# Kernel optimization log

Hardware: AMD Instinct MI355X
Metric: run time of the kernel (lower is better)

The kernel has to match this reference:

```python
import jax, jax.numpy as jnp
import numpy as np

B, N, K, S_IN, S_OUT, C, FD = 32, 325, 20, 12, 12, 10, 64
ALPHA = 0.5  # LeakyReLU negative slope

def leaky(x):
    return jnp.where(x >= 0, x, ALPHA * x)

def setup_inputs() -> dict:
    key = jax.random.key(0)
    ks = jax.random.split(key, 9)
    s = 0.2
    return {
        "fushed_features": jax.random.normal(ks[0], (B, N, FD), jnp.float32),
        "input_data": jax.random.normal(ks[1], (B, N, S_IN), jnp.float32),
        "w_W": jax.random.normal(ks[2], (S_IN, S_OUT), jnp.float32) * s,
        "w_b": jax.random.normal(ks[3], (S_OUT,), jnp.float32) * s,
        "a1_W": jax.random.normal(ks[4], (2 * S_OUT, 4 * S_OUT), jnp.float32) * s,
        "a1_b": jax.random.normal(ks[5], (4 * S_OUT,), jnp.float32) * s,
        "a2_W": jax.random.normal(ks[6], (4 * S_OUT, C), jnp.float32) * s,
        "a2_b": jax.random.normal(ks[7], (C,), jnp.float32) * s,
        "adj_mx_topk_index": jax.random.randint(ks[8], (B, N, K), 0, N),
    }

def reference(fushed_features, input_data, w_W, w_b, a1_W, a1_b, a2_W, a2_b, adj_mx_topk_index):
    # w_net: Linear + LeakyReLU -> wh [B,N,S_OUT]
    wh = leaky(input_data @ w_W + w_b)
    # a_net on cat([wh_i, wh_j]): split first linear to avoid materializing [B,N,N,2*S_OUT]
    hx = wh @ a1_W[:S_OUT]   # contribution of wh_x (row node i)
    hy = wh @ a1_W[S_OUT:]   # contribution of wh_y (col node j)
    hidden = leaky(hx[:, :, None, :] + hy[:, None, :, :] + a1_b)   # [B,N,N,4*S_OUT]
    attention = leaky(hidden @ a2_W + a2_b)                        # [B,N,N,C]
    idx = adj_mx_topk_index                                        # [B,N,K]
    # gather top-k neighbors along dim 2
    idx_c = jnp.broadcast_to(idx[..., None], idx.shape + (attention.shape[-1],))
    attention_mask = jnp.take_along_axis(attention, idx_c, axis=2)  # [B,N,K,C]
    attention_mask = jax.nn.softmax(attention_mask, axis=-1)
    # gather neighbor features: wh_expand_top_k[b,i,k] = wh[b, idx[b,i,k]]
    wh_topk = wh[jnp.arange(wh.shape[0])[:, None, None], idx]       # [B,N,K,S_OUT]
    # output = attention_mask^T @ wh_topk
    output_data = jnp.einsum('bnkc,bnks->bncs', attention_mask, wh_topk)
    # clustering loss on detached neighbor features (cosine similarity)
    wt = jax.lax.stop_gradient(wh_topk)
    wtn = wt / (jnp.linalg.norm(wt, axis=-1, keepdims=True) + 1e-8)
    dist_mat = jnp.einsum('bnks,bnls->bnkl', wtn, wtn)              # [B,N,K,K]
    same = (dist_mat >= 0.5).astype(dist_mat.dtype)
    diff = 1.0 - same
    prob = jnp.einsum('bnkc,bnlc->bnkl', attention_mask, attention_mask)
    prob = jnp.clip(prob, 1e-4, 1.0 - 1e-4)
    logp = jnp.log(prob)
    cl = -(same * logp - diff * logp)
    cluster_loss = (cl.sum((-1, -2)) - jnp.trace(cl, axis1=-2, axis2=-1)).mean()
    return output_data, cluster_loss, dist_mat.mean(), wh.mean()
```

## Files before the change

### kernel.cpp

```cpp
#include <hip/hip_runtime.h>
#include <math.h>

#define Bdim 32
#define Ndim 325
#define Kdim 20
#define Sdim 12
#define Cdim 10
#define Hdim 48
#define NB   (Bdim*Ndim)
#define OUT_SCALARS (NB*Cdim*Sdim)
#define Tpairs (Kdim*(Kdim-1)/2)

#define O_WH  0
#define O_HX  (O_WH + NB*Sdim)
#define O_HY  (O_HX + NB*Hdim)
#define O_PCL (O_HY + NB*Hdim)
#define O_PDS (O_PCL + NB)
#define O_PWH (O_PDS + NB)
#define WS_BASE_FLOATS (O_PWH + NB)

__device__ __forceinline__ float leaky(float x) { return x >= 0.f ? x : 0.5f * x; }

__global__ __launch_bounds__(256)
void node_kernel(const float* __restrict__ x,
                 const float* __restrict__ wW, const float* __restrict__ wb,
                 const float* __restrict__ A1, const float* __restrict__ b1,
                 float* __restrict__ ws)
{
    __shared__ float s_wh[4][Sdim];
    const int slot = threadIdx.x >> 6, lane = threadIdx.x & 63;
    const int node = blockIdx.x * 4 + slot;
    const float* xr = x + (size_t)node * Sdim;

    float v = 0.f;
    if (lane < Sdim) {
        float acc = wb[lane];
        #pragma unroll
        for (int i = 0; i < Sdim; i++) acc += xr[i] * wW[i * Sdim + lane];
        v = leaky(acc);
        s_wh[slot][lane] = v;
        ws[O_WH + (size_t)node * Sdim + lane] = v;
    }
    __syncthreads();

    #pragma unroll
    for (int rep = 0; rep < 2; rep++) {
        const int e = lane + rep * 64;
        if (e < 2 * Hdim) {
            const int which = e / Hdim, d = e - which * Hdim;
            float acc = which ? 0.f : b1[d];
            #pragma unroll
            for (int s = 0; s < Sdim; s++)
                acc += s_wh[slot][s] * A1[(which * Sdim + s) * Hdim + d];
            ws[(which ? O_HY : O_HX) + (size_t)node * Hdim + d] = acc;
        }
    }

    #pragma unroll
    for (int off = 32; off > 0; off >>= 1) v += __shfl_down(v, off);
    if (lane == 0) ws[O_PWH + node] = v;
}

__global__ __launch_bounds__(64)
void bn_kernel(const int* __restrict__ topk,
               const float* __restrict__ A2, const float* __restrict__ b2,
               float* __restrict__ ws, float* __restrict__ out)
{
    __shared__ float s_hxb[Hdim];
    __shared__ float s_A2[Hdim][12];
    __shared__ float s_whj[Kdim][20];
    __shared__ float s_wtn[Kdim][20];
    __shared__ float s_am [Kdim][12];
    __shared__ int   s_idx[Kdim];

    const int t = threadIdx.x, bn = blockIdx.x, b = bn / Ndim;

    if (t < Kdim) s_idx[t] = topk[(size_t)bn * Kdim + t];
    if (t < Hdim) s_hxb[t] = ws[O_HX + (size_t)bn * Hdim + t];
    for (int i = t; i < Hdim * 12; i += 64) {
        const int d = i / 12, c = i - d * 12;
        s_A2[d][c] = (c < Cdim) ? A2[d * Cdim + c] : 0.f;
    }
    __syncthreads();

    if (t < Kdim * 3) {
        const int k = t / 3, q = t - k * 3;
        const float4 v = *(const float4*)(ws + O_WH + ((size_t)b * Ndim + s_idx[k]) * Sdim + q * 4);
        *(float4*)&s_whj[k][q * 4] = v;
    }
    __syncthreads();

    float cl = 0.f, ds = 0.f;

    if (t < 2 * Kdim) {
        const int k = t >> 1, half = t & 1;
        const float4* hy4 = (const float4*)(ws + O_HY + ((size_t)b * Ndim + s_idx[k]) * Hdim) + half * 6;
        float acc[Cdim];
        #pragma unroll
        for (int c = 0; c < Cdim; c++) acc[c] = 0.f;
        #pragma unroll
        for (int q = 0; q < 6; q++) {
            const float4 hv = hy4[q];
            const float hvv[4] = { hv.x, hv.y, hv.z, hv.w };
            #pragma unroll
            for (int i = 0; i < 4; i++) {
                const int d = half * 24 + q * 4 + i;
                const float h = leaky(s_hxb[d] + hvv[i]);
                #pragma unroll
                for (int c = 0; c < Cdim; c++) acc[c] += h * s_A2[d][c];
            }
        }
        float full[Cdim];
        #pragma unroll
        for (int c = 0; c < Cdim; c++) full[c] = acc[c] + __shfl_xor(acc[c], 1);
        if (half == 0) {
            float m = -1e30f;
            #pragma unroll
            for (int c = 0; c < Cdim; c++) { full[c] = leaky(full[c] + b2[c]); m = fmaxf(m, full[c]); }
            float sum = 0.f;
            #pragma unroll
            for (int c = 0; c < Cdim; c++) { full[c] = __expf(full[c] - m); sum += full[c]; }
            const float inv = 1.f / sum;
            #pragma unroll
            for (int c = 0; c < Cdim; c++) s_am[k][c] = full[c] * inv;
            s_am[k][10] = 0.f; s_am[k][11] = 0.f;
        }
    } else if (t < 2 * Kdim + Kdim) {
        const int k = t - 2 * Kdim;
        const float4 w0 = *(const float4*)&s_whj[k][0];
        const float4 w1 = *(const float4*)&s_whj[k][4];
        const float4 w2 = *(const float4*)&s_whj[k][8];
        const float nn = w0.x*w0.x + w0.y*w0.y + w0.z*w0.z + w0.w*w0.w
                       + w1.x*w1.x + w1.y*w1.y + w1.z*w1.z + w1.w*w1.w
                       + w2.x*w2.x + w2.y*w2.y + w2.z*w2.z + w2.w*w2.w;
        const float invn = 1.f / (sqrtf(nn) + 1e-8f);
        *(float4*)&s_wtn[k][0] = make_float4(w0.x*invn, w0.y*invn, w0.z*invn, w0.w*invn);
        *(float4*)&s_wtn[k][4] = make_float4(w1.x*invn, w1.y*invn, w1.z*invn, w1.w*invn);
        *(float4*)&s_wtn[k][8] = make_float4(w2.x*invn, w2.y*invn, w2.z*invn, w2.w*invn);
        ds += nn * invn * invn;
    }
    __syncthreads();

    if (t < Cdim * 3) {
        const int c = t / 3, sq = t - c * 3;
        float4 o = make_float4(0.f, 0.f, 0.f, 0.f);
        #pragma unroll
        for (int k = 0; k < Kdim; k++) {
            const float a = s_am[k][c];
            const float4 w = *(const float4*)&s_whj[k][sq * 4];
            o.x += a * w.x; o.y += a * w.y; o.z += a * w.z; o.w += a * w.w;
        }
        *(float4*)(out + (size_t)bn * (Cdim * Sdim) + c * Sdim + sq * 4) = o;
    }

    #pragma unroll
    for (int it = 0; it < 3; it++) {
        const int e = t + it * 64;
        if (e < Tpairs) {
            const int r = Tpairs - 1 - e;
            const int m = (int)((sqrtf((float)(8 * r + 1)) - 1.f) * 0.5f + 1e-4f);
            const int k = Kdim - 2 - m;
            const int l = Kdim - 1 - (r - (m * (m + 1)) / 2);

            const float4 a0 = *(const float4*)&s_wtn[k][0];
            const float4 a1 = *(const float4*)&s_wtn[k][4];
            const float4 a2 = *(const float4*)&s_wtn[k][8];
            const float4 c0 = *(const float4*)&s_wtn[l][0];
            const float4 c1 = *(const float4*)&s_wtn[l][4];
            const float4 c2 = *(const float4*)&s_wtn[l][8];
            const float d = a0.x*c0.x + a0.y*c0.y + a0.z*c0.z + a0.w*c0.w
                          + a1.x*c1.x + a1.y*c1.y + a1.z*c1.z + a1.w*c1.w
                          + a2.x*c2.x + a2.y*c2.y + a2.z*c2.z + a2.w*c2.w;

            const float4 p0 = *(const float4*)&s_am[k][0];
            const float4 p1 = *(const float4*)&s_am[k][4];
            const float4 p2 = *(const float4*)&s_am[k][8];
            const float4 q0 = *(const float4*)&s_am[l][0];
            const float4 q1 = *(const float4*)&s_am[l][4];
            const float4 q2 = *(const float4*)&s_am[l][8];
            float p = p0.x*q0.x + p0.y*q0.y + p0.z*q0.z + p0.w*q0.w
                    + p1.x*q1.x + p1.y*q1.y + p1.z*q1.z + p1.w*q1.w
                    + p2.x*q2.x + p2.y*q2.y + p2.z*q2.z + p2.w*q2.w;

            p = fminf(fmaxf(p, 1e-4f), 1.f - 1e-4f);
            const float lp = __logf(p);
            ds += 2.f * d;
            cl += 2.f * ((d >= 0.5f) ? -lp : lp);
        }
    }

    #pragma unroll
    for (int off = 32; off > 0; off >>= 1) {
        cl += __shfl_down(cl, off);
        ds += __shfl_down(ds, off);
    }
    if (t == 0) { ws[O_PCL + bn] = cl; ws[O_PDS + bn] = ds; }
}

__global__ __launch_bounds__(1024)
void finalize(const float* __restrict__ ws, float* __restrict__ out)
{
    const int t = threadIdx.x;
    float cl = 0.f, ds = 0.f, wm = 0.f;
    for (int i = t; i < NB; i += 1024) {
        cl += ws[O_PCL + i]; ds += ws[O_PDS + i]; wm += ws[O_PWH + i];
    }
    #pragma unroll
    for (int off = 32; off > 0; off >>= 1) {
        cl += __shfl_down(cl, off);
        ds += __shfl_down(ds, off);
        wm += __shfl_down(wm, off);
    }
    __shared__ float r[3][16];
    const int w = t >> 6, lane = t & 63;
    if (lane == 0) { r[0][w] = cl; r[1][w] = ds; r[2][w] = wm; }
    __syncthreads();
    if (t == 0) {
        float c = 0.f, d = 0.f, m = 0.f;
        #pragma unroll
        for (int i = 0; i < 16; i++) { c += r[0][i]; d += r[1][i]; m += r[2][i]; }
        out[OUT_SCALARS + 0] = c * (1.f / (float)NB);
        out[OUT_SCALARS + 1] = d * (1.f / ((float)NB * Kdim * Kdim));
        out[OUT_SCALARS + 2] = m * (1.f / ((float)NB * Sdim));
    }
}

__global__ void zero_scalars(float* out) {
    const int t = threadIdx.x;
    if (t < 3) out[OUT_SCALARS + t] = 0.f;
}

__global__ __launch_bounds__(64)
void fused_kernel(const float* __restrict__ input_data,
                  const float* __restrict__ w_W,  const float* __restrict__ w_b,
                  const float* __restrict__ a1_W, const float* __restrict__ a1_b,
                  const float* __restrict__ a2_W, const float* __restrict__ a2_b,
                  const int*   __restrict__ topk,
                  float* __restrict__ out)
{
    __shared__ float s_wW[Sdim * Sdim];
    __shared__ float s_wb[Sdim];
    __shared__ float s_A1[2 * Sdim * Hdim];
    __shared__ float s_b1[Hdim];
    __shared__ float s_A2f[Hdim * Cdim];
    __shared__ float s_b2[Cdim];
    __shared__ float s_whs[Sdim];
    __shared__ float s_hx[Hdim];
    __shared__ float s_whj[Kdim][Sdim + 1];
    __shared__ float s_hid[Kdim][Hdim + 1];
    __shared__ float s_am [Kdim][Cdim + 1];
    __shared__ float s_wtn[Kdim][Sdim + 1];
    __shared__ int   s_idx[Kdim];

    const int t = threadIdx.x, bn = blockIdx.x, b = bn / Ndim;

    for (int i = t; i < Sdim * Sdim; i += 64)      s_wW[i] = w_W[i];
    if (t < Sdim)                                  s_wb[t] = w_b[t];
    for (int i = t; i < 2 * Sdim * Hdim; i += 64)  s_A1[i] = a1_W[i];
    if (t < Hdim)                                  s_b1[t] = a1_b[t];
    for (int i = t; i < Hdim * Cdim; i += 64)      s_A2f[i] = a2_W[i];
    if (t < Cdim)                                  s_b2[t] = a2_b[t];
    if (t < Kdim)                                  s_idx[t] = topk[(size_t)bn * Kdim + t];
    __syncthreads();

    const float* xs = input_data + (size_t)bn * Sdim;
    if (t < Sdim) {
        float acc = s_wb[t];
        #pragma unroll
        for (int i = 0; i < Sdim; i++) acc += xs[i] * s_wW[i * Sdim + t];
        s_whs[t] = leaky(acc);
    }
    __syncthreads();

    if (t < Hdim) {
        float acc = 0.f;
        #pragma unroll
        for (int s = 0; s < Sdim; s++) acc += s_whs[s] * s_A1[s * Hdim + t];
        s_hx[t] = acc;
    }
    for (int e = t; e < Kdim * Sdim; e += 64) {
        const int k = e / Sdim, ss = e - k * Sdim;
        const float* xj = input_data + ((size_t)b * Ndim + s_idx[k]) * Sdim;
        float acc = s_wb[ss];
        #pragma unroll
        for (int i = 0; i < Sdim; i++) acc += xj[i] * s_wW[i * Sdim + ss];
        s_whj[k][ss] = leaky(acc);
    }
    __syncthreads();

    for (int e = t; e < Kdim * Hdim; e += 64) {
        const int k = e / Hdim, d = e - k * Hdim;
        float acc = s_hx[d] + s_b1[d];
        #pragma unroll
        for (int s = 0; s < Sdim; s++) acc += s_whj[k][s] * s_A1[(Sdim + s) * Hdim + d];
        s_hid[k][d] = leaky(acc);
    }
    __syncthreads();

    for (int e = t; e < Kdim * Cdim; e += 64) {
        const int k = e / Cdim, c = e - k * Cdim;
        float acc = s_b2[c];
        #pragma unroll
        for (int d = 0; d < Hdim; d++) acc += s_hid[k][d] * s_A2f[d * Cdim + c];
        s_am[k][c] = leaky(acc);
    }
    __syncthreads();

    if (t < Kdim) {
        float m = -1e30f;
        #pragma unroll
        for (int c = 0; c < Cdim; c++) m = fmaxf(m, s_am[t][c]);
        float ex[Cdim]; float sum = 0.f;
        #pragma unroll
        for (int c = 0; c < Cdim; c++) { ex[c] = expf(s_am[t][c] - m); sum += ex[c]; }
        const float inv = 1.f / sum;
        #pragma unroll
        for (int c = 0; c < Cdim; c++) s_am[t][c] = ex[c] * inv;
        float nn = 0.f;
        #pragma unroll
        for (int s = 0; s < Sdim; s++) nn += s_whj[t][s] * s_whj[t][s];
        const float invn = 1.f / (sqrtf(nn) + 1e-8f);
        #pragma unroll
        for (int s = 0; s < Sdim; s++) s_wtn[t][s] = s_whj[t][s] * invn;
    }
    __syncthreads();

    float* op = out + (size_t)bn * (Cdim * Sdim);
    for (int e = t; e < Cdim * Sdim; e += 64) {
        const int c = e / Sdim, ss = e - c * Sdim;
        float acc = 0.f;
        #pragma unroll
        for (int k = 0; k < Kdim; k++) acc += s_am[k][c] * s_whj[k][ss];
        op[e] = acc;
    }

    float cl = 0.f, ds = 0.f;
    for (int e = t; e < Kdim * Kdim; e += 64) {
        const int k = e / Kdim, l = e - k * Kdim;
        float d = 0.f;
        #pragma unroll
        for (int s = 0; s < Sdim; s++) d += s_wtn[k][s] * s_wtn[l][s];
        ds += d;
        if (k != l) {
            float p = 0.f;
            #pragma unroll
            for (int c = 0; c < Cdim; c++) p += s_am[k][c] * s_am[l][c];
            p = fminf(fmaxf(p, 1e-4f), 1.f - 1e-4f);
            const float lp = logf(p);
            cl += (d >= 0.5f) ? -lp : lp;
        }
    }
    float whl = (t < Sdim) ? s_whs[t] : 0.f;
    #pragma unroll
    for (int off = 32; off > 0; off >>= 1) {
        cl  += __shfl_down(cl,  off);
        ds  += __shfl_down(ds,  off);
        whl += __shfl_down(whl, off);
    }
    if (t == 0) {
        atomicAdd(&out[OUT_SCALARS + 0], cl  * (1.f / (float)NB));
        atomicAdd(&out[OUT_SCALARS + 1], ds  * (1.f / ((float)NB * Kdim * Kdim)));
        atomicAdd(&out[OUT_SCALARS + 2], whl * (1.f / ((float)NB * Sdim)));
    }
}

extern "C" void kernel_launch(void* const* d_in, const int* in_sizes, int n_in,
                              void* d_out, int out_size, void* d_ws, size_t ws_size,
                              hipStream_t stream) {
    (void)in_sizes; (void)n_in; (void)out_size;
    const float* input_data = (const float*)d_in[1];
    const float* w_W  = (const float*)d_in[2];
    const float* w_b  = (const float*)d_in[3];
    const float* a1_W = (const float*)d_in[4];
    const float* a1_b = (const float*)d_in[5];
    const float* a2_W = (const float*)d_in[6];
    const float* a2_b = (const float*)d_in[7];
    const int*   topk = (const int*)d_in[8];
    float* out = (float*)d_out;
    float* ws  = (float*)d_ws;

    if (ws_size >= (size_t)WS_BASE_FLOATS * sizeof(float)) {
        hipLaunchKernelGGL(node_kernel, dim3(NB / 4), dim3(256), 0, stream,
                           input_data, w_W, w_b, a1_W, a1_b, ws);
        hipLaunchKernelGGL(bn_kernel, dim3(NB), dim3(64), 0, stream,
                           topk, a2_W, a2_b, ws, out);
        hipLaunchKernelGGL(finalize, dim3(1), dim3(1024), 0, stream, ws, out);
    } else {
        hipLaunchKernelGGL(zero_scalars, dim3(1), dim3(64), 0, stream, out);
        hipLaunchKernelGGL(fused_kernel, dim3(NB), dim3(64), 0, stream,
                           input_data, w_W, w_b, a1_W, a1_b, a2_W, a2_b, topk, out);
    }
}
```

Before: 113.3 us.

## Pack four nodes per bn_kernel block and fold finalize into last-block reduction

```diff
diff --git a/kernel.cpp b/kernel.cpp
--- a/kernel.cpp
+++ b/kernel.cpp
@@ -10,14 +10,16 @@
 #define NB   (Bdim*Ndim)
 #define OUT_SCALARS (NB*Cdim*Sdim)
 #define Tpairs (Kdim*(Kdim-1)/2)
+#define BN_BLOCKS (NB/4)
 
 #define O_WH  0
 #define O_HX  (O_WH + NB*Sdim)
 #define O_HY  (O_HX + NB*Hdim)
 #define O_PCL (O_HY + NB*Hdim)
-#define O_PDS (O_PCL + NB)
-#define O_PWH (O_PDS + NB)
-#define WS_BASE_FLOATS (O_PWH + NB)
+#define O_PDS (O_PCL + BN_BLOCKS)
+#define O_PWH (O_PDS + BN_BLOCKS)
+#define O_CNT (O_PWH + NB)
+#define WS_BASE_FLOATS (O_CNT + 4)
 
 __device__ __forceinline__ float leaky(float x) { return x >= 0.f ? x : 0.5f * x; }
 
@@ -32,6 +34,9 @@
     const int node = blockIdx.x * 4 + slot;
     const float* xr = x + (size_t)node * Sdim;
 
+    if (blockIdx.x == 0 && threadIdx.x == 0)
+        *(unsigned int*)(ws + O_CNT) = 0u;
+
     float v = 0.f;
     if (lane < Sdim) {
         float acc = wb[lane];
@@ -61,32 +66,39 @@
     if (lane == 0) ws[O_PWH + node] = v;
 }
 
-__global__ __launch_bounds__(64)
+__global__ __launch_bounds__(256)
 void bn_kernel(const int* __restrict__ topk,
                const float* __restrict__ A2, const float* __restrict__ b2,
                float* __restrict__ ws, float* __restrict__ out)
 {
-    __shared__ float s_hxb[Hdim];
     __shared__ float s_A2[Hdim][12];
-    __shared__ float s_whj[Kdim][20];
-    __shared__ float s_wtn[Kdim][20];
-    __shared__ float s_am [Kdim][12];
-    __shared__ int   s_idx[Kdim];
-
-    const int t = threadIdx.x, bn = blockIdx.x, b = bn / Ndim;
-
-    if (t < Kdim) s_idx[t] = topk[(size_t)bn * Kdim + t];
-    if (t < Hdim) s_hxb[t] = ws[O_HX + (size_t)bn * Hdim + t];
-    for (int i = t; i < Hdim * 12; i += 64) {
+    __shared__ float s_b2[Cdim];
+    __shared__ float s_hxb[4][Hdim];
+    __shared__ float s_whj[4][Kdim][12];
+    __shared__ float s_wtn[4][Kdim][12];
+    __shared__ float s_am [4][Kdim][12];
+    __shared__ int   s_idx[4][Kdim];
+    __shared__ float s_red[2][4];
+    __shared__ int   s_last;
+
+    const int tid = threadIdx.x;
+    const int slot = tid >> 6, t = tid & 63;
+    const int bn = blockIdx.x * 4 + slot, b = bn / Ndim;
+
+    for (int i = tid; i < Hdim * 12; i += 256) {
         const int d = i / 12, c = i - d * 12;
         s_A2[d][c] = (c < Cdim) ? A2[d * Cdim + c] : 0.f;
     }
+    if (tid < Cdim) s_b2[tid] = b2[tid];
+
+    if (t < Kdim) s_idx[slot][t] = topk[(size_t)bn * Kdim + t];
+    if (t < Hdim) s_hxb[slot][t] = ws[O_HX + (size_t)bn * Hdim + t];
     __syncthreads();
 
     if (t < Kdim * 3) {
         const int k = t / 3, q = t - k * 3;
-        const float4 v = *(const float4*)(ws + O_WH + ((size_t)b * Ndim + s_idx[k]) * Sdim + q * 4);
-        *(float4*)&s_whj[k][q * 4] = v;
+        const float4 v = *(const float4*)(ws + O_WH + ((size_t)b * Ndim + s_idx[slot][k]) * Sdim + q * 4);
+        *(float4*)&s_whj[slot][k][q * 4] = v;
     }
     __syncthreads();
 
@@ -94,7 +106,7 @@
 
     if (t < 2 * Kdim) {
         const int k = t >> 1, half = t & 1;
-        const float4* hy4 = (const float4*)(ws + O_HY + ((size_t)b * Ndim + s_idx[k]) * Hdim) + half * 6;
+        const float4* hy4 = (const float4*)(ws + O_HY + ((size_t)b * Ndim + s_idx[slot][k]) * Hdim) + half * 6;
         float acc[Cdim];
         #pragma unroll
         for (int c = 0; c < Cdim; c++) acc[c] = 0.f;
@@ -105,7 +117,7 @@
             #pragma unroll
             for (int i = 0; i < 4; i++) {
                 const int d = half * 24 + q * 4 + i;
-                const float h = leaky(s_hxb[d] + hvv[i]);
+                const float h = leaky(s_hxb[slot][d] + hvv[i]);
                 #pragma unroll
                 for (int c = 0; c < Cdim; c++) acc[c] += h * s_A2[d][c];
             }
@@ -116,27 +128,27 @@
         if (half == 0) {
             float m = -1e30f;
             #pragma unroll
-            for (int c = 0; c < Cdim; c++) { full[c] = leaky(full[c] + b2[c]); m = fmaxf(m, full[c]); }
+            for (int c = 0; c < Cdim; c++) { full[c] = leaky(full[c] + s_b2[c]); m = fmaxf(m, full[c]); }
             float sum = 0.f;
             #pragma unroll
             for (int c = 0; c < Cdim; c++) { full[c] = __expf(full[c] - m); sum += full[c]; }
             const float inv = 1.f / sum;
             #pragma unroll
-            for (int c = 0; c < Cdim; c++) s_am[k][c] = full[c] * inv;
-            s_am[k][10] = 0.f; s_am[k][11] = 0.f;
+            for (int c = 0; c < Cdim; c++) s_am[slot][k][c] = full[c] * inv;
+            s_am[slot][k][10] = 0.f; s_am[slot][k][11] = 0.f;
         }
     } else if (t < 2 * Kdim + Kdim) {
         const int k = t - 2 * Kdim;
-        const float4 w0 = *(const float4*)&s_whj[k][0];
-        const float4 w1 = *(const float4*)&s_whj[k][4];
-        const float4 w2 = *(const float4*)&s_whj[k][8];
+        const float4 w0 = *(const float4*)&s_whj[slot][k][0];
+        const float4 w1 = *(const float4*)&s_whj[slot][k][4];
+        const float4 w2 = *(const float4*)&s_whj[slot][k][8];
         const float nn = w0.x*w0.x + w0.y*w0.y + w0.z*w0.z + w0.w*w0.w
                        + w1.x*w1.x + w1.y*w1.y + w1.z*w1.z + w1.w*w1.w
                        + w2.x*w2.x + w2.y*w2.y + w2.z*w2.z + w2.w*w2.w;
         const float invn = 1.f / (sqrtf(nn) + 1e-8f);
-        *(float4*)&s_wtn[k][0] = make_float4(w0.x*invn, w0.y*invn, w0.z*invn, w0.w*invn);
-        *(float4*)&s_wtn[k][4] = make_float4(w1.x*invn, w1.y*invn, w1.z*invn, w1.w*invn);
-        *(float4*)&s_wtn[k][8] = make_float4(w2.x*invn, w2.y*invn, w2.z*invn, w2.w*invn);
+        *(float4*)&s_wtn[slot][k][0] = make_float4(w0.x*invn, w0.y*invn, w0.z*invn, w0.w*invn);
+        *(float4*)&s_wtn[slot][k][4] = make_float4(w1.x*invn, w1.y*invn, w1.z*invn, w1.w*invn);
+        *(float4*)&s_wtn[slot][k][8] = make_float4(w2.x*invn, w2.y*invn, w2.z*invn, w2.w*invn);
         ds += nn * invn * invn;
     }
     __syncthreads();
@@ -146,8 +158,8 @@
         float4 o = make_float4(0.f, 0.f, 0.f, 0.f);
         #pragma unroll
         for (int k = 0; k < Kdim; k++) {
-            const float a = s_am[k][c];
-            const float4 w = *(const float4*)&s_whj[k][sq * 4];
+            const float a = s_am[slot][k][c];
+            const float4 w = *(const float4*)&s_whj[slot][k][sq * 4];
             o.x += a * w.x; o.y += a * w.y; o.z += a * w.z; o.w += a * w.w;
         }
         *(float4*)(out + (size_t)bn * (Cdim * Sdim) + c * Sdim + sq * 4) = o;
@@ -162,22 +174,22 @@
             const int k = Kdim - 2 - m;
             const int l = Kdim - 1 - (r - (m * (m + 1)) / 2);
 
-            const float4 a0 = *(const float4*)&s_wtn[k][0];
-            const float4 a1 = *(const float4*)&s_wtn[k][4];
-            const float4 a2 = *(const float4*)&s_wtn[k][8];
-            const float4 c0 = *(const float4*)&s_wtn[l][0];
-            const float4 c1 = *(const float4*)&s_wtn[l][4];
-            const float4 c2 = *(const float4*)&s_wtn[l][8];
+            const float4 a0 = *(const float4*)&s_wtn[slot][k][0];
+            const float4 a1 = *(const float4*)&s_wtn[slot][k][4];
+            const float4 a2 = *(const float4*)&s_wtn[slot][k][8];
+            const float4 c0 = *(const float4*)&s_wtn[slot][l][0];
+            const float4 c1 = *(const float4*)&s_wtn[slot][l][4];
+            const float4 c2 = *(const float4*)&s_wtn[slot][l][8];
             const float d = a0.x*c0.x + a0.y*c0.y + a0.z*c0.z + a0.w*c0.w
                           + a1.x*c1.x + a1.y*c1.y + a1.z*c1.z + a1.w*c1.w
                           + a2.x*c2.x + a2.y*c2.y + a2.z*c2.z + a2.w*c2.w;
 
-            const float4 p0 = *(const float4*)&s_am[k][0];
-            const float4 p1 = *(const float4*)&s_am[k][4];
-            const float4 p2 = *(const float4*)&s_am[k][8];
-            const float4 q0 = *(const float4*)&s_am[l][0];
-            const float4 q1 = *(const float4*)&s_am[l][4];
-            const float4 q2 = *(const float4*)&s_am[l][8];
+            const float4 p0 = *(const float4*)&s_am[slot][k][0];
+            const float4 p1 = *(const float4*)&s_am[slot][k][4];
+            const float4 p2 = *(const float4*)&s_am[slot][k][8];
+            const float4 q0 = *(const float4*)&s_am[slot][l][0];
+            const float4 q1 = *(const float4*)&s_am[slot][l][4];
+            const float4 q2 = *(const float4*)&s_am[slot][l][8];
             float p = p0.x*q0.x + p0.y*q0.y + p0.z*q0.z + p0.w*q0.w
                     + p1.x*q1.x + p1.y*q1.y + p1.z*q1.z + p1.w*q1.w
                     + p2.x*q2.x + p2.y*q2.y + p2.z*q2.z + p2.w*q2.w;
@@ -194,34 +206,39 @@
         cl += __shfl_down(cl, off);
         ds += __shfl_down(ds, off);
     }
-    if (t == 0) { ws[O_PCL + bn] = cl; ws[O_PDS + bn] = ds; }
-}
-
-__global__ __launch_bounds__(1024)
-void finalize(const float* __restrict__ ws, float* __restrict__ out)
-{
-    const int t = threadIdx.x;
-    float cl = 0.f, ds = 0.f, wm = 0.f;
-    for (int i = t; i < NB; i += 1024) {
-        cl += ws[O_PCL + i]; ds += ws[O_PDS + i]; wm += ws[O_PWH + i];
-    }
-    #pragma unroll
-    for (int off = 32; off > 0; off >>= 1) {
-        cl += __shfl_down(cl, off);
-        ds += __shfl_down(ds, off);
-        wm += __shfl_down(wm, off);
-    }
-    __shared__ float r[3][16];
-    const int w = t >> 6, lane = t & 63;
-    if (lane == 0) { r[0][w] = cl; r[1][w] = ds; r[2][w] = wm; }
-    __syncthreads();
-    if (t == 0) {
-        float c = 0.f, d = 0.f, m = 0.f;
-        #pragma unroll
-        for (int i = 0; i < 16; i++) { c += r[0][i]; d += r[1][i]; m += r[2][i]; }
-        out[OUT_SCALARS + 0] = c * (1.f / (float)NB);
-        out[OUT_SCALARS + 1] = d * (1.f / ((float)NB * Kdim * Kdim));
-        out[OUT_SCALARS + 2] = m * (1.f / ((float)NB * Sdim));
+    if (t == 0) { s_red[0][slot] = cl; s_red[1][slot] = ds; }
+    __syncthreads();
+    if (tid == 0) {
+        ws[O_PCL + blockIdx.x] = s_red[0][0] + s_red[0][1] + s_red[0][2] + s_red[0][3];
+        ws[O_PDS + blockIdx.x] = s_red[1][0] + s_red[1][1] + s_red[1][2] + s_red[1][3];
+        __threadfence();
+        const unsigned old = atomicAdd((unsigned int*)(ws + O_CNT), 1u);
+        s_last = (old == (unsigned)(gridDim.x - 1));
+    }
+    __syncthreads();
+
+    if (s_last) {
+        __threadfence();
+        float fcl = 0.f, fds = 0.f, fwm = 0.f;
+        for (int i = tid; i < BN_BLOCKS; i += 256) { fcl += ws[O_PCL + i]; fds += ws[O_PDS + i]; }
+        for (int i = tid; i < NB; i += 256) fwm += ws[O_PWH + i];
+        #pragma unroll
+        for (int off = 32; off > 0; off >>= 1) {
+            fcl += __shfl_down(fcl, off);
+            fds += __shfl_down(fds, off);
+            fwm += __shfl_down(fwm, off);
+        }
+        __shared__ float fr[3][4];
+        if (t == 0) { fr[0][slot] = fcl; fr[1][slot] = fds; fr[2][slot] = fwm; }
+        __syncthreads();
+        if (tid == 0) {
+            const float c = fr[0][0] + fr[0][1] + fr[0][2] + fr[0][3];
+            const float d = fr[1][0] + fr[1][1] + fr[1][2] + fr[1][3];
+            const float m = fr[2][0] + fr[2][1] + fr[2][2] + fr[2][3];
+            out[OUT_SCALARS + 0] = c * (1.f / (float)NB);
+            out[OUT_SCALARS + 1] = d * (1.f / ((float)NB * Kdim * Kdim));
+            out[OUT_SCALARS + 2] = m * (1.f / ((float)NB * Sdim));
+        }
     }
 }
 
@@ -243,7 +260,7 @@
     __shared__ float s_A1[2 * Sdim * Hdim];
     __shared__ float s_b1[Hdim];
     __shared__ float s_A2f[Hdim * Cdim];
-    __shared__ float s_b2[Cdim];
+    __shared__ float s_b2f[Cdim];
     __shared__ float s_whs[Sdim];
     __shared__ float s_hx[Hdim];
     __shared__ float s_whj[Kdim][Sdim + 1];
@@ -259,7 +276,7 @@
     for (int i = t; i < 2 * Sdim * Hdim; i += 64)  s_A1[i] = a1_W[i];
     if (t < Hdim)                                  s_b1[t] = a1_b[t];
     for (int i = t; i < Hdim * Cdim; i += 64)      s_A2f[i] = a2_W[i];
-    if (t < Cdim)                                  s_b2[t] = a2_b[t];
+    if (t < Cdim)                                  s_b2f[t] = a2_b[t];
     if (t < Kdim)                                  s_idx[t] = topk[(size_t)bn * Kdim + t];
     __syncthreads();
 
@@ -299,7 +316,7 @@
 
     for (int e = t; e < Kdim * Cdim; e += 64) {
         const int k = e / Cdim, c = e - k * Cdim;
-        float acc = s_b2[c];
+        float acc = s_b2f[c];
         #pragma unroll
         for (int d = 0; d < Hdim; d++) acc += s_hid[k][d] * s_A2f[d * Cdim + c];
         s_am[k][c] = leaky(acc);
@@ -382,9 +399,8 @@
     if (ws_size >= (size_t)WS_BASE_FLOATS * sizeof(float)) {
         hipLaunchKernelGGL(node_kernel, dim3(NB / 4), dim3(256), 0, stream,
                            input_data, w_W, w_b, a1_W, a1_b, ws);
-        hipLaunchKernelGGL(bn_kernel, dim3(NB), dim3(64), 0, stream,
+        hipLaunchKernelGGL(bn_kernel, dim3(BN_BLOCKS), dim3(256), 0, stream,
                            topk, a2_W, a2_b, ws, out);
-        hipLaunchKernelGGL(finalize, dim3(1), dim3(1024), 0, stream, ws, out);
     } else {
         hipLaunchKernelGGL(zero_scalars, dim3(1), dim3(64), 0, stream, out);
         hipLaunchKernelGGL(fused_kernel, dim3(NB), dim3(64), 0, stream,
```

Measured after the change: 170.4 us. 50.4% more time.
